# Performance work log

Hardware: AMD Instinct MI355X
Metric: run time of the kernel (lower is better)

Reference implementation:

```python
import jax, jax.numpy as jnp
import numpy as np
from jax.scipy.special import logsumexp
from jax import lax

TARGET_SIZE = 50
TAG_SIZE = TARGET_SIZE + 2  # +2 for START/END tags


def setup_inputs() -> dict:
    key = jax.random.key(0)
    k1, k2 = jax.random.split(key)
    B, L, T = 1024, 512, TAG_SIZE
    feats = jax.random.normal(k1, (B, L, T), dtype=jnp.float32)
    mask = jnp.ones((B, L), dtype=jnp.int32)
    # transitions init per CRF.__init__: zeros, with transitions[:, START]=-1000
    # and transitions[END, :]=-1000 (START=T-2, END=T-1). Add small noise to the
    # trainable part so gradients are non-trivial.
    trans = 0.1 * jax.random.normal(k2, (T, T), dtype=jnp.float32)
    trans = trans.at[:, T - 2].set(-1000.0)  # nothing transitions INTO start
    trans = trans.at[T - 1, :].set(-1000.0)  # nothing transitions OUT of end
    return {"feats": feats, "mask": mask, "transitions": trans}


def reference(feats, mask, transitions):
    # feats: (B, L, T), mask: (B, L) int, transitions: (T, T)
    B, L, T = feats.shape
    START, END = T - 2, T - 1
    # scores[t, b, i, j] = feats[b, t, j] + transitions[i, j]
    # initial partition = scores[0, :, START, :]
    partition0 = feats[:, 0, :] + transitions[START, :]  # (B, T)

    feats_t = jnp.swapaxes(feats[:, 1:, :], 0, 1)   # (L-1, B, T)
    mask_t = jnp.swapaxes(mask[:, 1:], 0, 1)        # (L-1, B)

    def step(part, xs):
        f_t, m_t = xs  # (B, T), (B,)
        # cur[b, i, j] = feats[b,t,j] + transitions[i,j] + partition[b,i]
        cur = f_t[:, None, :] + transitions[None, :, :] + part[:, :, None]
        cur_part = logsumexp(cur, axis=1)  # reduce over previous tag i -> (B, T)
        part = jnp.where((m_t > 0)[:, None], cur_part, part)
        return part, None

    partition, _ = lax.scan(step, partition0, (feats_t, mask_t))

    # final transition step, then select END tag
    final_vals = transitions[None, :, :] + partition[:, :, None]  # (B, T, T)
    final_partition = logsumexp(final_vals, axis=1)[:, END]       # (B,)
    return final_partition.sum()
```

## Files before the change

### kernel.cpp

```cpp
#include <hip/hip_runtime.h>


#define TT 52
#define LL 512
#define NS 8
#define KSPLIT 256

typedef float v2f __attribute__((ext_vector_type(2)));

__device__ __forceinline__ v2f pkfma(v2f a, v2f b, v2f c) {
#if __has_builtin(__builtin_elementwise_fma)
    return __builtin_elementwise_fma(a, b, c);
#else
    v2f r; r.x = fmaf(a.x, b.x, c.x); r.y = fmaf(a.y, b.y, c.y); return r;
#endif
}

__device__ __forceinline__ float rl(float x, int lane) {
    return __int_as_float(__builtin_amdgcn_readlane(__float_as_int(x), lane));
}

__device__ __forceinline__ float matvec52(const float4* pq, const v2f* E2) {
    v2f ae0 = {0.f, 0.f}, ae1 = {0.f, 0.f};
    v2f ao0 = {0.f, 0.f}, ao1 = {0.f, 0.f};
#pragma unroll
    for (int kq = 0; kq < TT / 4; ++kq) {
        float4 q = pq[kq];
        v2f lo = {q.x, q.y};
        v2f hi = {q.z, q.w};
        if ((kq & 1) == 0) {
            ae0 = pkfma(lo, E2[2 * kq + 0], ae0);
            ae1 = pkfma(hi, E2[2 * kq + 1], ae1);
        } else {
            ao0 = pkfma(lo, E2[2 * kq + 0], ao0);
            ao1 = pkfma(hi, E2[2 * kq + 1], ao1);
        }
    }
    v2f s = (ae0 + ao0) + (ae1 + ao1);
    return s.x + s.y;
}

__global__ void __launch_bounds__(128)
__attribute__((amdgpu_waves_per_eu(2, 2)))
crf_fwd(
    const float* __restrict__ feats,
    const int*   __restrict__ mask,
    const float* __restrict__ trans,
    float*       __restrict__ out)
{
    __shared__ __align__(16) float plds[2][64];
    __shared__ float shsh[2];

    const int b   = blockIdx.x;
    const int tid = threadIdx.x;
    const int w   = tid >> 6;
    const int j   = tid & 63;
    const bool act = (j < TT);
    const int jc = act ? j : 0;

    const float* fb = feats + (size_t)b * LL * TT;
    const int*   mb = mask  + (size_t)b * LL;

    float pv;
    float shift;

    if (w == 0) {
        v2f E2[TT / 2];
#pragma unroll
        for (int k = 0; k < TT / 2; ++k) {
            float e0 = __expf(trans[(2 * k + 0) * TT + jc]);
            float e1 = __expf(trans[(2 * k + 1) * TT + jc]);
            E2[k].x = act ? e0 : 0.0f;
            E2[k].y = act ? e1 : 0.0f;
        }

        float part0 = act ? (fb[j] + trans[(TT - 2) * TT + j]) : -1.0e30f;
        shift = rl(part0, 0);
        pv = act ? __expf(part0 - shift) : 0.0f;
        plds[0][j] = pv;

        const float4* pq = (const float4*)plds[0];

        float fA[NS], fB[NS]; int mA[NS], mB[NS];
#pragma unroll
        for (int u = 0; u < NS; ++u) {
            fA[u] = fb[(1 + u) * TT + jc];
            mA[u] = mb[1 + u];
        }

        auto fwd_group = [&](float (&fp)[NS], int (&mc)[NS],
                             float (&fn)[NS], int (&mn)[NS], int t0) {
#pragma unroll
            for (int u = 0; u < NS; ++u) {
                int tn = t0 + NS + u;
                fn[u] = fb[tn * TT + jc];
                mn[u] = mb[tn];
            }
            float ef[NS];
#pragma unroll
            for (int u = 0; u < NS; ++u) ef[u] = __expf(fp[u]);
#pragma unroll
            for (int u = 0; u < NS; ++u) {
                float pn = matvec52(pq, E2) * ef[u];
                pv = (mc[u] > 0) ? pn : pv;
                if (u == NS - 1) {
                    float c = rl(pv, 0);
                    shift += __logf(c);
                    pv *= __builtin_amdgcn_rcpf(c);
                }
                plds[0][j] = pv;
            }
        };

        for (int t0 = 1; t0 <= 241; t0 += 2 * NS) {
            fwd_group(fA, mA, fB, mB, t0);
            fwd_group(fB, mB, fA, mA, t0 + NS);
        }
    } else {
        v2f E2[TT / 2];
#pragma unroll
        for (int k = 0; k < TT / 2; ++k) {
            float e0 = __expf(trans[jc * TT + 2 * k + 0]);
            float e1 = __expf(trans[jc * TT + 2 * k + 1]);
            E2[k].x = act ? e0 : 0.0f;
            E2[k].y = act ? e1 : 0.0f;
        }

        pv = act ? __expf(trans[jc * TT + (TT - 1)]) : 0.0f;
        shift = 0.0f;

        const float4* pq = (const float4*)plds[1];

        float fA[NS], fB[NS]; int mA[NS], mB[NS];
#pragma unroll
        for (int u = 0; u < NS; ++u) {
            fA[u] = fb[(LL - 1 - u) * TT + jc];
            mA[u] = mb[LL - 1 - u];
        }

        auto bwd_group = [&](float (&fp)[NS], int (&mc)[NS],
                             float (&fn)[NS], int (&mn)[NS], int g) {
#pragma unroll
            for (int u = 0; u < NS; ++u) {
                int kn = g + NS + u;
                fn[u] = fb[(LL - 1 - kn) * TT + jc];
                mn[u] = mb[LL - 1 - kn];
            }
            float ef[NS];
#pragma unroll
            for (int u = 0; u < NS; ++u) ef[u] = __expf(fp[u]);
#pragma unroll
            for (int u = 0; u < NS; ++u) {
                plds[1][j] = ef[u] * pv;
                float pn = matvec52(pq, E2);
                pv = (mc[u] > 0) ? pn : pv;
                if (u == NS - 1) {
                    float c = rl(pv, 0);
                    shift += __logf(c);
                    pv *= __builtin_amdgcn_rcpf(c);
                }
            }
        };

        for (int g = 0; g <= 224; g += 2 * NS) {
            bwd_group(fA, mA, fB, mB, g);
            bwd_group(fB, mB, fA, mA, g + NS);
        }
        bwd_group(fA, mA, fB, mB, 240);

#pragma unroll
        for (int u = 0; u < 7; ++u) {
            float efu = __expf(fB[u]);
            plds[1][j] = efu * pv;
            float pn = matvec52(pq, E2);
            pv = (mB[u] > 0) ? pn : pv;
        }

        {
            float c = rl(pv, 0);
            shift += __logf(c);
            pv *= __builtin_amdgcn_rcpf(c);
        }
    }

    plds[w][j] = pv;
    if (j == 0) shsh[w] = shift;
    __syncthreads();

    if (w == 0) {
        float wj  = plds[1][j];
        float val = act ? (pv * wj) : 0.0f;
#pragma unroll
        for (int o = 32; o >= 1; o >>= 1)
            val += __shfl_xor(val, o, 64);
        if (j == 0) atomicAdd(out, __logf(val) + shift + shsh[1]);
    }
}

extern "C" void kernel_launch(void* const* d_in, const int* in_sizes, int n_in,
                              void* d_out, int out_size, void* d_ws, size_t ws_size,
                              hipStream_t stream) {
    const float* feats = (const float*)d_in[0];
    const int*   mask  = (const int*)d_in[1];
    const float* trans = (const float*)d_in[2];
    float* out = (float*)d_out;

    const int B = in_sizes[1] / LL;

    hipMemsetAsync(d_out, 0, sizeof(float), stream);
    crf_fwd<<<B, 128, 0, stream>>>(feats, mask, trans, out);
}
```

Baseline: 200.9 us.

## Split CRF matvec reduction across wave halves with permlane32 swap

Each lane now reads only half of the partition vector from LDS (28 entries) and computes partial dot products for both its own output tag and its partner's tag in the other half-wave. The partials are exchanged with permlane32_swap (or a shuffle as fallback) and summed. The aim is to halve LDS reads per step on the serial recurrence. In exchange each step gains a cross-lane swap and the lane holds twice as many exp(transition) registers for its half.

```diff
diff --git a/kernel.cpp b/kernel.cpp
--- a/kernel.cpp
+++ b/kernel.cpp
@@ -4,9 +4,9 @@
 #define TT 52
 #define LL 512
 #define NS 8
-#define KSPLIT 256
 
 typedef float v2f __attribute__((ext_vector_type(2)));
+typedef unsigned int uv2 __attribute__((ext_vector_type(2)));
 
 __device__ __forceinline__ v2f pkfma(v2f a, v2f b, v2f c) {
 #if __has_builtin(__builtin_elementwise_fma)
@@ -20,24 +20,35 @@
     return __int_as_float(__builtin_amdgcn_readlane(__float_as_int(x), lane));
 }
 
-__device__ __forceinline__ float matvec52(const float4* pq, const v2f* E2) {
-    v2f ae0 = {0.f, 0.f}, ae1 = {0.f, 0.f};
-    v2f ao0 = {0.f, 0.f}, ao1 = {0.f, 0.f};
-#pragma unroll
-    for (int kq = 0; kq < TT / 4; ++kq) {
-        float4 q = pq[kq];
-        v2f lo = {q.x, q.y};
-        v2f hi = {q.z, q.w};
-        if ((kq & 1) == 0) {
-            ae0 = pkfma(lo, E2[2 * kq + 0], ae0);
-            ae1 = pkfma(hi, E2[2 * kq + 1], ae1);
-        } else {
-            ao0 = pkfma(lo, E2[2 * kq + 0], ao0);
-            ao1 = pkfma(hi, E2[2 * kq + 1], ao1);
-        }
-    }
-    v2f s = (ae0 + ao0) + (ae1 + ao1);
-    return s.x + s.y;
+__device__ __forceinline__ float xhalf(float v, bool hlo) {
+#if __has_builtin(__builtin_amdgcn_permlane32_swap)
+    uv2 r = __builtin_amdgcn_permlane32_swap(__float_as_uint(v),
+                                             __float_as_uint(v), false, false);
+    return hlo ? __uint_as_float(r.y) : __uint_as_float(r.x);
+#else
+    return __shfl_xor(v, 32, 64);
+#endif
+}
+
+__device__ __forceinline__ float matvec52h(const float4* pqh, const v2f* Ea,
+                                           const v2f* Eb, bool hlo) {
+    v2f a0 = {0.f, 0.f}, a1 = {0.f, 0.f};
+    v2f b0 = {0.f, 0.f}, b1 = {0.f, 0.f};
+#pragma unroll
+    for (int q = 0; q < 7; ++q) {
+        float4 Q = pqh[q];
+        v2f lo = {Q.x, Q.y};
+        v2f hi = {Q.z, Q.w};
+        a0 = pkfma(lo, Ea[2 * q + 0], a0);
+        a1 = pkfma(hi, Ea[2 * q + 1], a1);
+        b0 = pkfma(lo, Eb[2 * q + 0], b0);
+        b1 = pkfma(hi, Eb[2 * q + 1], b1);
+    }
+    v2f s1 = a0 + a1;
+    v2f s2 = b0 + b1;
+    float P1 = s1.x + s1.y;
+    float P2 = s2.x + s2.y;
+    return P1 + xhalf(P2, hlo);
 }
 
 __global__ void __launch_bounds__(128)
@@ -55,6 +66,10 @@
     const int tid = threadIdx.x;
     const int w   = tid >> 6;
     const int j   = tid & 63;
+    const int h   = j >> 5;
+    const bool hlo = (h == 0);
+    const int jx  = j ^ 32;
+    const int i0  = 28 * h;
     const bool act = (j < TT);
     const int jc = act ? j : 0;
 
@@ -64,23 +79,47 @@
     float pv;
     float shift;
 
+    v2f Ea[14], Eb[14];
     if (w == 0) {
-        v2f E2[TT / 2];
-#pragma unroll
-        for (int k = 0; k < TT / 2; ++k) {
-            float e0 = __expf(trans[(2 * k + 0) * TT + jc]);
-            float e1 = __expf(trans[(2 * k + 1) * TT + jc]);
-            E2[k].x = act ? e0 : 0.0f;
-            E2[k].y = act ? e1 : 0.0f;
-        }
-
+#pragma unroll
+        for (int k = 0; k < 14; ++k) {
+            int ia = i0 + 2 * k, ib = ia + 1;
+            int iac = ia < TT ? ia : 0, ibc = ib < TT ? ib : 0;
+            int jcc = jc, jxc = jx < TT ? jx : 0;
+            float eax = __expf(trans[iac * TT + jcc]);
+            float eay = __expf(trans[ibc * TT + jcc]);
+            float ebx = __expf(trans[iac * TT + jxc]);
+            float eby = __expf(trans[ibc * TT + jxc]);
+            Ea[k].x = (ia < TT && j  < TT) ? eax : 0.0f;
+            Ea[k].y = (ib < TT && j  < TT) ? eay : 0.0f;
+            Eb[k].x = (ia < TT && jx < TT) ? ebx : 0.0f;
+            Eb[k].y = (ib < TT && jx < TT) ? eby : 0.0f;
+        }
+    } else {
+#pragma unroll
+        for (int k = 0; k < 14; ++k) {
+            int ia = i0 + 2 * k, ib = ia + 1;
+            int iac = ia < TT ? ia : 0, ibc = ib < TT ? ib : 0;
+            int jcc = jc, jxc = jx < TT ? jx : 0;
+            float eax = __expf(trans[jcc * TT + iac]);
+            float eay = __expf(trans[jcc * TT + ibc]);
+            float ebx = __expf(trans[jxc * TT + iac]);
+            float eby = __expf(trans[jxc * TT + ibc]);
+            Ea[k].x = (ia < TT && j  < TT) ? eax : 0.0f;
+            Ea[k].y = (ib < TT && j  < TT) ? eay : 0.0f;
+            Eb[k].x = (ia < TT && jx < TT) ? ebx : 0.0f;
+            Eb[k].y = (ib < TT && jx < TT) ? eby : 0.0f;
+        }
+    }
+
+    const float4* pqh = ((const float4*)plds[w]) + 7 * h;
+
+    if (w == 0) {
         float part0 = act ? (fb[j] + trans[(TT - 2) * TT + j]) : -1.0e30f;
         shift = rl(part0, 0);
         pv = act ? __expf(part0 - shift) : 0.0f;
         plds[0][j] = pv;
 
-        const float4* pq = (const float4*)plds[0];
-
         float fA[NS], fB[NS]; int mA[NS], mB[NS];
 #pragma unroll
         for (int u = 0; u < NS; ++u) {
@@ -101,7 +140,7 @@
             for (int u = 0; u < NS; ++u) ef[u] = __expf(fp[u]);
 #pragma unroll
             for (int u = 0; u < NS; ++u) {
-                float pn = matvec52(pq, E2) * ef[u];
+                float pn = matvec52h(pqh, Ea, Eb, hlo) * ef[u];
                 pv = (mc[u] > 0) ? pn : pv;
                 if (u == NS - 1) {
                     float c = rl(pv, 0);
@@ -117,19 +156,8 @@
             fwd_group(fB, mB, fA, mA, t0 + NS);
         }
     } else {
-        v2f E2[TT / 2];
-#pragma unroll
-        for (int k = 0; k < TT / 2; ++k) {
-            float e0 = __expf(trans[jc * TT + 2 * k + 0]);
-            float e1 = __expf(trans[jc * TT + 2 * k + 1]);
-            E2[k].x = act ? e0 : 0.0f;
-            E2[k].y = act ? e1 : 0.0f;
-        }
-
         pv = act ? __expf(trans[jc * TT + (TT - 1)]) : 0.0f;
         shift = 0.0f;
-
-        const float4* pq = (const float4*)plds[1];
 
         float fA[NS], fB[NS]; int mA[NS], mB[NS];
 #pragma unroll
@@ -152,7 +180,7 @@
 #pragma unroll
             for (int u = 0; u < NS; ++u) {
                 plds[1][j] = ef[u] * pv;
-                float pn = matvec52(pq, E2);
+                float pn = matvec52h(pqh, Ea, Eb, hlo);
                 pv = (mc[u] > 0) ? pn : pv;
                 if (u == NS - 1) {
                     float c = rl(pv, 0);
@@ -172,7 +200,7 @@
         for (int u = 0; u < 7; ++u) {
             float efu = __expf(fB[u]);
             plds[1][j] = efu * pv;
-            float pn = matvec52(pq, E2);
+            float pn = matvec52h(pqh, Ea, Eb, hlo);
             pv = (mB[u] > 0) ? pn : pv;
         }
 
```

Measured after the change: 200.6 us. About the same (-0.1%).

## Replace LDS-based matvec with register reduce-scatter using DPP cross-lane ops

Applied to the files above, without the earlier changes.

Each step's 52x52 matrix-vector product now uses a register-only reduce-scatter. Every lane multiplies its own partition value by a permuted column of exp(transitions), then the products are summed across lanes with DPP swaps, a shuffle and permlane32 swap. Tags are remapped through a bit permutation (tau/rho) so the reduced output lands on the right lane. This removes the per-step LDS write and the 13 float4 LDS reads, trading them for 64 multiplies and a longer chain of cross-lane adds. The extra work per step and the serial reduction depth could outweigh the saved LDS latency.

```diff
diff --git a/kernel.cpp b/kernel.cpp
--- a/kernel.cpp
+++ b/kernel.cpp
@@ -4,40 +4,59 @@
 #define TT 52
 #define LL 512
 #define NS 8
-#define KSPLIT 256
 
 typedef float v2f __attribute__((ext_vector_type(2)));
-
-__device__ __forceinline__ v2f pkfma(v2f a, v2f b, v2f c) {
-#if __has_builtin(__builtin_elementwise_fma)
-    return __builtin_elementwise_fma(a, b, c);
-#else
-    v2f r; r.x = fmaf(a.x, b.x, c.x); r.y = fmaf(a.y, b.y, c.y); return r;
-#endif
-}
+typedef unsigned int uv2 __attribute__((ext_vector_type(2)));
 
 __device__ __forceinline__ float rl(float x, int lane) {
     return __int_as_float(__builtin_amdgcn_readlane(__float_as_int(x), lane));
 }
 
-__device__ __forceinline__ float matvec52(const float4* pq, const v2f* E2) {
-    v2f ae0 = {0.f, 0.f}, ae1 = {0.f, 0.f};
-    v2f ao0 = {0.f, 0.f}, ao1 = {0.f, 0.f};
-#pragma unroll
-    for (int kq = 0; kq < TT / 4; ++kq) {
-        float4 q = pq[kq];
-        v2f lo = {q.x, q.y};
-        v2f hi = {q.z, q.w};
-        if ((kq & 1) == 0) {
-            ae0 = pkfma(lo, E2[2 * kq + 0], ae0);
-            ae1 = pkfma(hi, E2[2 * kq + 1], ae1);
-        } else {
-            ao0 = pkfma(lo, E2[2 * kq + 0], ao0);
-            ao1 = pkfma(hi, E2[2 * kq + 1], ao1);
-        }
-    }
-    v2f s = (ae0 + ao0) + (ae1 + ao1);
-    return s.x + s.y;
+template <int CTRL, int M>
+__device__ __forceinline__ float dppx(float v) {
+#if __has_builtin(__builtin_amdgcn_update_dpp)
+    return __int_as_float(__builtin_amdgcn_update_dpp(
+        0, __float_as_int(v), CTRL, 0xF, 0xF, true));
+#else
+    return __shfl_xor(v, M, 64);
+#endif
+}
+
+__device__ __forceinline__ float xhalf(float v, bool hlo) {
+#if __has_builtin(__builtin_amdgcn_permlane32_swap)
+    uv2 r = __builtin_amdgcn_permlane32_swap(__float_as_uint(v),
+                                             __float_as_uint(v), false, false);
+    return hlo ? __uint_as_float(r.y) : __uint_as_float(r.x);
+#else
+    return __shfl_xor(v, 32, 64);
+#endif
+}
+
+constexpr int rho(int r) {
+    return ((r >> 5) & 1) | (((r >> 4) & 1) << 1) | (((r >> 3) & 1) << 3) |
+           (((r >> 2) & 1) << 2) | (((r >> 1) & 1) << 4) | ((r & 1) << 5);
+}
+
+__device__ __forceinline__ float rsmv(float x, const v2f* C2, bool hlo) {
+    float P[64];
+#pragma unroll
+    for (int k = 0; k < 32; ++k) {
+        v2f xx; xx.x = x; xx.y = x;
+        v2f pr = xx * C2[k];
+        P[2 * k] = pr.x; P[2 * k + 1] = pr.y;
+    }
+#pragma unroll
+    for (int r = 0; r < 32; ++r) P[r] += dppx<0xB1, 1>(P[r + 32]);
+#pragma unroll
+    for (int r = 0; r < 16; ++r) P[r] += dppx<0x4E, 2>(P[r + 16]);
+#pragma unroll
+    for (int r = 0; r < 8; ++r)  P[r] += dppx<0x128, 8>(P[r + 8]);
+#pragma unroll
+    for (int r = 0; r < 4; ++r)  P[r] += dppx<0x140, 15>(P[r + 4]);
+#pragma unroll
+    for (int r = 0; r < 2; ++r)  P[r] += __shfl_xor(P[r + 2], 16, 64);
+    P[0] += xhalf(P[1], hlo);
+    return P[0];
 }
 
 __global__ void __launch_bounds__(128)
@@ -48,15 +67,17 @@
     const float* __restrict__ trans,
     float*       __restrict__ out)
 {
-    __shared__ __align__(16) float plds[2][64];
+    __shared__ float plds[2][64];
     __shared__ float shsh[2];
 
     const int b   = blockIdx.x;
     const int tid = threadIdx.x;
     const int w   = tid >> 6;
     const int j   = tid & 63;
+    const bool hlo = (j < 32);
+    const int tau = (j & 4) ? (j ^ 11) : j;
     const bool act = (j < TT);
-    const int jc = act ? j : 0;
+    const int tc = act ? tau : 0;
 
     const float* fb = feats + (size_t)b * LL * TT;
     const int*   mb = mask  + (size_t)b * LL;
@@ -64,27 +85,34 @@
     float pv;
     float shift;
 
+    v2f C2[32];
+#pragma unroll
+    for (int k = 0; k < 32; ++k) {
+        int c0 = rho(2 * k) ^ tau;
+        int c1 = rho(2 * k + 1) ^ tau;
+        int c0c = c0 < TT ? c0 : 0;
+        int c1c = c1 < TT ? c1 : 0;
+        float e0, e1;
+        if (w == 0) {
+            e0 = __expf(trans[tc * TT + c0c]);
+            e1 = __expf(trans[tc * TT + c1c]);
+        } else {
+            e0 = __expf(trans[c0c * TT + tc]);
+            e1 = __expf(trans[c1c * TT + tc]);
+        }
+        C2[k].x = (act && c0 < TT) ? e0 : 0.0f;
+        C2[k].y = (act && c1 < TT) ? e1 : 0.0f;
+    }
+
     if (w == 0) {
-        v2f E2[TT / 2];
-#pragma unroll
-        for (int k = 0; k < TT / 2; ++k) {
-            float e0 = __expf(trans[(2 * k + 0) * TT + jc]);
-            float e1 = __expf(trans[(2 * k + 1) * TT + jc]);
-            E2[k].x = act ? e0 : 0.0f;
-            E2[k].y = act ? e1 : 0.0f;
-        }
-
-        float part0 = act ? (fb[j] + trans[(TT - 2) * TT + j]) : -1.0e30f;
+        float part0 = act ? (fb[tau] + trans[(TT - 2) * TT + tau]) : -1.0e30f;
         shift = rl(part0, 0);
         pv = act ? __expf(part0 - shift) : 0.0f;
-        plds[0][j] = pv;
-
-        const float4* pq = (const float4*)plds[0];
 
         float fA[NS], fB[NS]; int mA[NS], mB[NS];
 #pragma unroll
         for (int u = 0; u < NS; ++u) {
-            fA[u] = fb[(1 + u) * TT + jc];
+            fA[u] = fb[(1 + u) * TT + tc];
             mA[u] = mb[1 + u];
         }
 
@@ -93,7 +121,7 @@
 #pragma unroll
             for (int u = 0; u < NS; ++u) {
                 int tn = t0 + NS + u;
-                fn[u] = fb[tn * TT + jc];
+                fn[u] = fb[tn * TT + tc];
                 mn[u] = mb[tn];
             }
             float ef[NS];
@@ -101,14 +129,13 @@
             for (int u = 0; u < NS; ++u) ef[u] = __expf(fp[u]);
 #pragma unroll
             for (int u = 0; u < NS; ++u) {
-                float pn = matvec52(pq, E2) * ef[u];
+                float pn = rsmv(pv, C2, hlo) * ef[u];
                 pv = (mc[u] > 0) ? pn : pv;
                 if (u == NS - 1) {
                     float c = rl(pv, 0);
                     shift += __logf(c);
                     pv *= __builtin_amdgcn_rcpf(c);
                 }
-                plds[0][j] = pv;
             }
         };
 
@@ -117,24 +144,13 @@
             fwd_group(fB, mB, fA, mA, t0 + NS);
         }
     } else {
-        v2f E2[TT / 2];
-#pragma unroll
-        for (int k = 0; k < TT / 2; ++k) {
-            float e0 = __expf(trans[jc * TT + 2 * k + 0]);
-            float e1 = __expf(trans[jc * TT + 2 * k + 1]);
-            E2[k].x = act ? e0 : 0.0f;
-            E2[k].y = act ? e1 : 0.0f;
-        }
-
-        pv = act ? __expf(trans[jc * TT + (TT - 1)]) : 0.0f;
+        pv = act ? __expf(trans[tc * TT + (TT - 1)]) : 0.0f;
         shift = 0.0f;
 
-        const float4* pq = (const float4*)plds[1];
-
         float fA[NS], fB[NS]; int mA[NS], mB[NS];
 #pragma unroll
         for (int u = 0; u < NS; ++u) {
-            fA[u] = fb[(LL - 1 - u) * TT + jc];
+            fA[u] = fb[(LL - 1 - u) * TT + tc];
             mA[u] = mb[LL - 1 - u];
         }
 
@@ -143,7 +159,7 @@
 #pragma unroll
             for (int u = 0; u < NS; ++u) {
                 int kn = g + NS + u;
-                fn[u] = fb[(LL - 1 - kn) * TT + jc];
+                fn[u] = fb[(LL - 1 - kn) * TT + tc];
                 mn[u] = mb[LL - 1 - kn];
             }
             float ef[NS];
@@ -151,8 +167,7 @@
             for (int u = 0; u < NS; ++u) ef[u] = __expf(fp[u]);
 #pragma unroll
             for (int u = 0; u < NS; ++u) {
-                plds[1][j] = ef[u] * pv;
-                float pn = matvec52(pq, E2);
+                float pn = rsmv(ef[u] * pv, C2, hlo);
                 pv = (mc[u] > 0) ? pn : pv;
                 if (u == NS - 1) {
                     float c = rl(pv, 0);
@@ -170,9 +185,7 @@
 
 #pragma unroll
         for (int u = 0; u < 7; ++u) {
-            float efu = __expf(fB[u]);
-            plds[1][j] = efu * pv;
-            float pn = matvec52(pq, E2);
+            float pn = rsmv(__expf(fB[u]) * pv, C2, hlo);
             pv = (mB[u] > 0) ? pn : pv;
         }
 
```

New measurement: 242.9 us. +20.9%, slower.
